# Performance work log

Hardware: AMD Instinct MI355X
Metric: run time of the kernel (lower is better)

The kernel has to match this reference:

```python
import jax, jax.numpy as jnp
import numpy as np

N_BINS = 10  # rho thresholds 0.1..0.9 -> bin ids 0..9

def setup_inputs() -> dict:
    key = jax.random.key(0)
    k1, k2, k3 = jax.random.split(key, 3)
    B, D, G = 4_000_000, 11, 10
    z_1 = jax.random.uniform(k1, (B, D), dtype=jnp.float32)
    z_2 = jax.random.uniform(k2, (B, D), dtype=jnp.float32)
    dist_grade = jax.random.uniform(k3, (B, G), dtype=jnp.float32)
    return {"z_1": z_1, "z_2": z_2, "dist_grade": dist_grade}

def reference(z_1, z_2, dist_grade):
    # to_center: (x1, x2) columns -> center coords proxy, shape [2, B]
    dx = z_2[:, 0] - z_1[:, 0]
    dy = -(z_2[:, 2] - z_1[:, 2])  # dir_vec[1] = -dir_vec[1]
    rho = jnp.sqrt(dx * dx + dy * dy)  # [B]
    # threshold binning: dist_id = #{k in 1..9 : rho >= k/10}
    thresholds = jnp.arange(1, N_BINS, dtype=jnp.float32) * 0.1  # [9]
    dist_id = jnp.sum(rho[:, None] >= thresholds[None, :], axis=-1).astype(jnp.int32)  # [B]
    # one-hot scatter then weighted sum == gather along bins
    out = jnp.take_along_axis(dist_grade, dist_id[:, None], axis=1)[:, 0]  # [B]
    return out
```

## Files before the change

### kernel.cpp

```cpp
#include <hip/hip_runtime.h>


#define ZD 11
#define GD 10
#define ROWS 256

__global__ __launch_bounds__(256) void rho_valuation_kernel(
    const float* __restrict__ z1,
    const float* __restrict__ z2,
    const float* __restrict__ dg,
    float* __restrict__ out,
    int B)
{
    __shared__ float s_z1[ROWS * ZD];
    __shared__ float s_z2[ROWS * ZD];
    __shared__ float s_dg[ROWS * GD];

    const int t = threadIdx.x;
    const long base = (long)blockIdx.x * ROWS;

    if (base + ROWS <= B) {
        const float4* g1 = (const float4*)(z1 + base * ZD);
        const float4* g2 = (const float4*)(z2 + base * ZD);
        const float4* g3 = (const float4*)(dg + base * GD);
        float4* l1 = (float4*)s_z1;
        float4* l2 = (float4*)s_z2;
        float4* l3 = (float4*)s_dg;

        #pragma unroll
        for (int i = 0; i < 3; ++i) {
            int idx = t + i * 256;
            if (idx < (ROWS * ZD) / 4) { l1[idx] = g1[idx]; l2[idx] = g2[idx]; }
        }
        #pragma unroll
        for (int i = 0; i < 3; ++i) {
            int idx = t + i * 256;
            if (idx < (ROWS * GD) / 4) { l3[idx] = g3[idx]; }
        }
        __syncthreads();

        float a0 = s_z1[t * ZD + 0];
        float a2 = s_z1[t * ZD + 2];
        float c0 = s_z2[t * ZD + 0];
        float c2 = s_z2[t * ZD + 2];

        float dx = __fadd_rn(c0, -a0);
        float dy = __fadd_rn(a2, -c2);
        float s   = __fadd_rn(__fmul_rn(dx, dx), __fmul_rn(dy, dy));
        float rho = __fsqrt_rn(s);

        int id = 0;
        #pragma unroll
        for (int k = 1; k <= 9; ++k)
            id += (rho >= (float)k * 0.1f) ? 1 : 0;

        out[base + t] = s_dg[t * GD + id];
    } else {
        long b = base + t;
        if (b < B) {
            float a0 = z1[b * ZD + 0];
            float a2 = z1[b * ZD + 2];
            float c0 = z2[b * ZD + 0];
            float c2 = z2[b * ZD + 2];
            float dx = __fadd_rn(c0, -a0);
            float dy = __fadd_rn(a2, -c2);
            float s   = __fadd_rn(__fmul_rn(dx, dx), __fmul_rn(dy, dy));
            float rho = __fsqrt_rn(s);
            int id = 0;
            #pragma unroll
            for (int k = 1; k <= 9; ++k)
                id += (rho >= (float)k * 0.1f) ? 1 : 0;
            out[b] = dg[b * GD + id];
        }
    }
}

extern "C" void kernel_launch(void* const* d_in, const int* in_sizes, int n_in,
                              void* d_out, int out_size, void* d_ws, size_t ws_size,
                              hipStream_t stream) {
    const float* z1 = (const float*)d_in[0];
    const float* z2 = (const float*)d_in[1];
    const float* dg = (const float*)d_in[2];
    float* out = (float*)d_out;

    int B = out_size;
    const int block = ROWS;
    int grid = (B + block - 1) / block;
    rho_valuation_kernel<<<grid, block, 0, stream>>>(z1, z2, dg, out, B);
}
```

Baseline: 432.0 us.

## Replace LDS staging with direct strided loads in a grid-stride loop

Drops the shared-memory staging that copied every row of z_1, z_2 and dist_grade in full. Instead, each thread loads only the four needed elements and the single selected dist_grade value straight from global memory. It uses a fixed 1024-block grid-stride loop with 5 independent rows per iteration to keep many loads in flight. This cuts requested bytes but relies on scattered 4-byte accesses whose cache-line footprint may still cover most of the data.

Measured after the change: 444.9 us. +3.0%, slower.

```diff
diff --git a/kernel.cpp b/kernel.cpp
--- a/kernel.cpp
+++ b/kernel.cpp
@@ -3,7 +3,19 @@
 
 #define ZD 11
 #define GD 10
-#define ROWS 256
+
+__device__ __forceinline__ int rho_bin(float a0, float a2, float c0, float c2)
+{
+    float dx  = __fadd_rn(c0, -a0);
+    float dy  = __fadd_rn(a2, -c2);
+    float s   = __fadd_rn(__fmul_rn(dx, dx), __fmul_rn(dy, dy));
+    float rho = __fsqrt_rn(s);
+    int id = 0;
+    #pragma unroll
+    for (int k = 1; k <= 9; ++k)
+        id += (rho >= (float)k * 0.1f) ? 1 : 0;
+    return id;
+}
 
 __global__ __launch_bounds__(256) void rho_valuation_kernel(
     const float* __restrict__ z1,
@@ -12,66 +24,47 @@
     float* __restrict__ out,
     int B)
 {
-    __shared__ float s_z1[ROWS * ZD];
-    __shared__ float s_z2[ROWS * ZD];
-    __shared__ float s_dg[ROWS * GD];
+    const int T = gridDim.x * blockDim.x;
+    int i = blockIdx.x * blockDim.x + threadIdx.x;
 
-    const int t = threadIdx.x;
-    const long base = (long)blockIdx.x * ROWS;
+    for (; i + 4 * T < B; i += 5 * T) {
+        const int r0 = i, r1 = i + T, r2 = i + 2 * T, r3 = i + 3 * T, r4 = i + 4 * T;
+        const int o0 = r0 * ZD, o1 = r1 * ZD, o2 = r2 * ZD, o3 = r3 * ZD, o4 = r4 * ZD;
 
-    if (base + ROWS <= B) {
-        const float4* g1 = (const float4*)(z1 + base * ZD);
-        const float4* g2 = (const float4*)(z2 + base * ZD);
-        const float4* g3 = (const float4*)(dg + base * GD);
-        float4* l1 = (float4*)s_z1;
-        float4* l2 = (float4*)s_z2;
-        float4* l3 = (float4*)s_dg;
+        float a0_0 = z1[o0],     a2_0 = z1[o0 + 2];
+        float a0_1 = z1[o1],     a2_1 = z1[o1 + 2];
+        float a0_2 = z1[o2],     a2_2 = z1[o2 + 2];
+        float a0_3 = z1[o3],     a2_3 = z1[o3 + 2];
+        float a0_4 = z1[o4],     a2_4 = z1[o4 + 2];
+        float c0_0 = z2[o0],     c2_0 = z2[o0 + 2];
+        float c0_1 = z2[o1],     c2_1 = z2[o1 + 2];
+        float c0_2 = z2[o2],     c2_2 = z2[o2 + 2];
+        float c0_3 = z2[o3],     c2_3 = z2[o3 + 2];
+        float c0_4 = z2[o4],     c2_4 = z2[o4 + 2];
 
-        #pragma unroll
-        for (int i = 0; i < 3; ++i) {
-            int idx = t + i * 256;
-            if (idx < (ROWS * ZD) / 4) { l1[idx] = g1[idx]; l2[idx] = g2[idx]; }
-        }
-        #pragma unroll
-        for (int i = 0; i < 3; ++i) {
-            int idx = t + i * 256;
-            if (idx < (ROWS * GD) / 4) { l3[idx] = g3[idx]; }
-        }
-        __syncthreads();
+        const int id0 = rho_bin(a0_0, a2_0, c0_0, c2_0);
+        const int id1 = rho_bin(a0_1, a2_1, c0_1, c2_1);
+        const int id2 = rho_bin(a0_2, a2_2, c0_2, c2_2);
+        const int id3 = rho_bin(a0_3, a2_3, c0_3, c2_3);
+        const int id4 = rho_bin(a0_4, a2_4, c0_4, c2_4);
 
-        float a0 = s_z1[t * ZD + 0];
-        float a2 = s_z1[t * ZD + 2];
-        float c0 = s_z2[t * ZD + 0];
-        float c2 = s_z2[t * ZD + 2];
+        float g0 = dg[r0 * GD + id0];
+        float g1 = dg[r1 * GD + id1];
+        float g2 = dg[r2 * GD + id2];
+        float g3 = dg[r3 * GD + id3];
+        float g4 = dg[r4 * GD + id4];
 
-        float dx = __fadd_rn(c0, -a0);
-        float dy = __fadd_rn(a2, -c2);
-        float s   = __fadd_rn(__fmul_rn(dx, dx), __fmul_rn(dy, dy));
-        float rho = __fsqrt_rn(s);
+        out[r0] = g0;
+        out[r1] = g1;
+        out[r2] = g2;
+        out[r3] = g3;
+        out[r4] = g4;
+    }
 
-        int id = 0;
-        #pragma unroll
-        for (int k = 1; k <= 9; ++k)
-            id += (rho >= (float)k * 0.1f) ? 1 : 0;
-
-        out[base + t] = s_dg[t * GD + id];
-    } else {
-        long b = base + t;
-        if (b < B) {
-            float a0 = z1[b * ZD + 0];
-            float a2 = z1[b * ZD + 2];
-            float c0 = z2[b * ZD + 0];
-            float c2 = z2[b * ZD + 2];
-            float dx = __fadd_rn(c0, -a0);
-            float dy = __fadd_rn(a2, -c2);
-            float s   = __fadd_rn(__fmul_rn(dx, dx), __fmul_rn(dy, dy));
-            float rho = __fsqrt_rn(s);
-            int id = 0;
-            #pragma unroll
-            for (int k = 1; k <= 9; ++k)
-                id += (rho >= (float)k * 0.1f) ? 1 : 0;
-            out[b] = dg[b * GD + id];
-        }
+    for (; i < B; i += T) {
+        const int o = i * ZD;
+        const int id = rho_bin(z1[o], z1[o + 2], z2[o], z2[o + 2]);
+        out[i] = dg[i * GD + id];
     }
 }
 
@@ -84,7 +77,9 @@
     float* out = (float*)d_out;
 
     int B = out_size;
-    const int block = ROWS;
-    int grid = (B + block - 1) / block;
+    const int block = 256;
+    int grid = 1024;
+    int max_grid = (B + block - 1) / block;
+    if (grid > max_grid) grid = max_grid;
     rho_valuation_kernel<<<grid, block, 0, stream>>>(z1, z2, dg, out, B);
 }
```
